# Optimization experiments

Measured on AMD Instinct MI355X. Metric: run time of the kernel, lower is better.

The kernel has to match this reference:

```python
import jax, jax.numpy as jnp
import numpy as np
from jax import lax

TSTEPS = 20
THRES = 1.0
DECAY = (2**4 - 1) / 2**4  # 0.9375


def _avgpool2(x):
    # (C,H,W) -> (C,H/2,W/2), AvgPool2d(2)
    C, H, W = x.shape
    return x.reshape(C, H // 2, 2, W // 2, 2).mean(axis=(2, 4))


def _conv(s, w):
    # s: (Cin,H,W), w: (Cout,Cin,k,k), VALID conv
    return lax.conv_general_dilated(
        s[None], w, (1, 1), 'VALID',
        dimension_numbers=('NCHW', 'OIHW', 'NCHW'))[0]


def setup_inputs() -> dict:
    key = jax.random.key(0)
    k0, k1, k2, k3, k4 = jax.random.split(key, 5)
    image = jax.random.uniform(k0, (3, 128, 128), dtype=jnp.float32)
    # kaiming_normal: std = sqrt(2/fan_in)
    w_c1 = jax.random.normal(k1, (32, 3, 5, 5), dtype=jnp.float32) * np.sqrt(2.0 / (3 * 25))
    w_c2 = jax.random.normal(k2, (64, 32, 5, 5), dtype=jnp.float32) * np.sqrt(2.0 / (32 * 25))
    w_l1 = jax.random.normal(k3, (512, 200704), dtype=jnp.float32) * np.sqrt(2.0 / 200704)
    w_l2 = jax.random.normal(k4, (10, 512), dtype=jnp.float32) * np.sqrt(2.0 / 512)
    return {"image": image, "w_c1": w_c1, "w_c2": w_c2, "w_l1": w_l1, "w_l2": w_l2}


def _lif(mempot, drive):
    # membrane update for conv/linear layers: integrate, fire, reset, decay
    mp = mempot + drive
    spk = (mp >= THRES).astype(mp.dtype)
    mp = (mp - THRES * spk) * ((1.0 - spk) * DECAY + spk)
    return mp, spk


def reference(image, w_c1, w_c2, w_l1, w_l2):
    img = _avgpool2(image)  # (3,64,64)
    f32 = jnp.float32
    carry0 = (
        jnp.zeros((3, 64, 64), f32),    # mempot input
        jnp.zeros((32, 60, 60), f32),   # mempot conv1
        jnp.zeros((64, 56, 56), f32),   # mempot conv2
        jnp.zeros((512,), f32),         # mempot linear1
        jnp.zeros((10,), f32),          # mempot linear2
        jnp.zeros((32, 60, 60), f32),   # conv1 spikes from previous step
        jnp.zeros((64, 56, 56), f32),   # conv2 spikes from previous step
        jnp.zeros((512,), f32),         # linear1 spikes from previous step
    )

    def step(carry, _):
        mp_in, mp_c1, mp_c2, mp_l1, mp_l2, sp_c1, sp_c2, sp_l1 = carry
        # input layer: integrate-and-fire, no decay
        mp_in = mp_in + img
        s_in = (mp_in >= THRES).astype(f32)
        mp_in = mp_in - THRES * s_in
        # conv1 consumes current input spikes
        mp_c1, ns_c1 = _lif(mp_c1, _conv(s_in, w_c1))
        # conv2 consumes conv1 spikes from previous timestep
        mp_c2, ns_c2 = _lif(mp_c2, _conv(sp_c1, w_c2))
        # flatten consumes conv2 spikes from previous timestep
        s_f = sp_c2.reshape(-1)  # (200704,)
        mp_l1, ns_l1 = _lif(mp_l1, w_l1 @ s_f)
        # linear2 consumes linear1 spikes from previous timestep
        mp_l2, ns_l2 = _lif(mp_l2, w_l2 @ sp_l1)
        return (mp_in, mp_c1, mp_c2, mp_l1, mp_l2, ns_c1, ns_c2, ns_l1), ns_l2

    _, out = lax.scan(step, carry0, None, length=TSTEPS)
    # original returns spikes of shape (tsteps+1, 10); row 0 stays zero
    return jnp.concatenate([jnp.zeros((1, 10), f32), out], axis=0)
```

## Files before the change

### kernel.cpp

```cpp
#include <hip/hip_runtime.h>
#include <hip/hip_bf16.h>

#define THRES 1.0f
#define DECAY 0.9375f

#define OFF_SIN    0u
#define OFF_D1     245760u
#define OFF_SC1    2549760u
#define OFF_D2     4853760u
#define OFF_MASK   8667136u
#define OFF_PART   8867840u
#define OFF_Z      8935936u

__global__ void k_input(const float* __restrict__ image, float* __restrict__ s_in) {
    int idx = blockIdx.x * 256 + threadIdx.x;
    if (idx >= 12288) return;
    int c = idx >> 12;
    int p = idx & 4095;
    int y = p >> 6, x = p & 63;
    const float* b = image + c * 16384 + (2 * y) * 128 + 2 * x;
    float v = ((b[0] + b[1]) + (b[128] + b[129])) * 0.25f;
    float mp = 0.f;
    for (int t = 0; t < 20; ++t) {
        mp += v;
        float s = (mp >= THRES) ? 1.f : 0.f;
        s_in[t * 12288 + idx] = s;
        mp -= s;
    }
}

__global__ void k_conv1(const float* __restrict__ s_in, const float* __restrict__ w_c1,
                        float* __restrict__ D1) {
    int task = blockIdx.x * 256 + threadIdx.x;
    if (task >= 57600) return;
    int xc = task % 6;
    int tmp = task / 6;
    int y = tmp % 60; tmp /= 60;
    int og = tmp % 8;
    int t  = tmp / 8;
    int o0 = og * 4, x0 = xc * 10;
    float acc[4][10];
    #pragma unroll
    for (int o = 0; o < 4; ++o)
        #pragma unroll
        for (int x = 0; x < 10; ++x) acc[o][x] = 0.f;
    const float* inb = s_in + t * 12288;
    for (int c = 0; c < 3; ++c)
        for (int ky = 0; ky < 5; ++ky) {
            float in[14];
            const float* row = inb + c * 4096 + (y + ky) * 64 + x0;
            #pragma unroll
            for (int i = 0; i < 14; ++i) in[i] = row[i];
            #pragma unroll
            for (int kx = 0; kx < 5; ++kx)
                #pragma unroll
                for (int o = 0; o < 4; ++o) {
                    float w = w_c1[((o0 + o) * 3 + c) * 25 + ky * 5 + kx];
                    #pragma unroll
                    for (int x = 0; x < 10; ++x) acc[o][x] += in[x + kx] * w;
                }
        }
    #pragma unroll
    for (int o = 0; o < 4; ++o)
        #pragma unroll
        for (int x = 0; x < 10; ++x)
            D1[((t * 32 + o0 + o) * 60 + y) * 60 + x0 + x] = acc[o][x];
}

__global__ void k_lif1(const float* __restrict__ D1, float* __restrict__ s_c1) {
    int idx = blockIdx.x * 256 + threadIdx.x;
    if (idx >= 115200) return;
    float mp = 0.f;
    for (int t = 0; t < 20; ++t) {
        mp += D1[t * 115200 + idx];
        float s = (mp >= THRES) ? 1.f : 0.f;
        s_c1[t * 115200 + idx] = s;
        mp = (s != 0.f) ? (mp - THRES) : mp * DECAY;
    }
}

__global__ void k_conv2(const float* __restrict__ s_c1, const float* __restrict__ w_c2,
                        float* __restrict__ D2) {
    int task = blockIdx.x * 256 + threadIdx.x;
    if (task >= 119168) return;
    int xc = task % 7;
    int tmp = task / 7;
    int y = tmp % 56; tmp /= 56;
    int og = tmp % 16;
    int tp = tmp / 16;
    int o0 = og * 4, x0 = xc * 8;
    float acc[4][8];
    #pragma unroll
    for (int o = 0; o < 4; ++o)
        #pragma unroll
        for (int x = 0; x < 8; ++x) acc[o][x] = 0.f;
    const float* inb = s_c1 + tp * 115200;
    for (int c = 0; c < 32; ++c)
        #pragma unroll
        for (int ky = 0; ky < 5; ++ky) {
            float in[12];
            const float* row = inb + c * 3600 + (y + ky) * 60 + x0;
            #pragma unroll
            for (int i = 0; i < 12; ++i) in[i] = row[i];
            #pragma unroll
            for (int kx = 0; kx < 5; ++kx)
                #pragma unroll
                for (int o = 0; o < 4; ++o) {
                    float w = w_c2[((o0 + o) * 32 + c) * 25 + ky * 5 + kx];
                    #pragma unroll
                    for (int x = 0; x < 8; ++x) acc[o][x] += in[x + kx] * w;
                }
        }
    #pragma unroll
    for (int o = 0; o < 4; ++o)
        #pragma unroll
        for (int x = 0; x < 8; ++x)
            D2[((tp * 64 + o0 + o) * 56 + y) * 56 + x0 + x] = acc[o][x];
}

__global__ void k_lif2(const float* __restrict__ D2, unsigned int* __restrict__ mask) {
    int idx = blockIdx.x * 256 + threadIdx.x;
    if (idx >= 200704) return;
    float mp = 0.f;
    unsigned int m = 0u;
    for (int u = 1; u < 20; ++u) {
        mp += D2[(u - 1) * 200704 + idx];
        float s = (mp >= THRES) ? 1.f : 0.f;
        if (s != 0.f) m |= (1u << u);
        mp = (s != 0.f) ? (mp - THRES) : mp * DECAY;
    }
    mask[idx] = m;
}

__global__ void __launch_bounds__(256) k_gemm(const float* __restrict__ W,
                                              const unsigned int* __restrict__ mask,
                                              float* __restrict__ partials) {
    int rg = blockIdx.x / 7, js = blockIdx.x % 7;
    int i0 = rg * 4;
    size_t j0 = (size_t)js * 28672;
    int tid = threadIdx.x;
    float acc[4][19];
    #pragma unroll
    for (int r = 0; r < 4; ++r)
        #pragma unroll
        for (int t = 0; t < 19; ++t) acc[r][t] = 0.f;

    const float* W0 = W + (size_t)(i0 + 0) * 200704 + j0;
    const float* W1 = W + (size_t)(i0 + 1) * 200704 + j0;
    const float* W2 = W + (size_t)(i0 + 2) * 200704 + j0;
    const float* W3 = W + (size_t)(i0 + 3) * 200704 + j0;
    const unsigned int* M = mask + j0;

    for (int it = 0; it < 28; ++it) {
        int j = (it * 256 + tid) * 4;
        uint4  m4 = *(const uint4*)(M + j);
        float4 a0 = *(const float4*)(W0 + j);
        float4 a1 = *(const float4*)(W1 + j);
        float4 a2 = *(const float4*)(W2 + j);
        float4 a3 = *(const float4*)(W3 + j);
        unsigned int mm[4] = {m4.x, m4.y, m4.z, m4.w};
        float w0a[4] = {a0.x, a0.y, a0.z, a0.w};
        float w1a[4] = {a1.x, a1.y, a1.z, a1.w};
        float w2a[4] = {a2.x, a2.y, a2.z, a2.w};
        float w3a[4] = {a3.x, a3.y, a3.z, a3.w};
        #pragma unroll
        for (int jj = 0; jj < 4; ++jj) {
            unsigned int m = mm[jj];
            float v0 = w0a[jj], v1 = w1a[jj], v2 = w2a[jj], v3 = w3a[jj];
            #pragma unroll
            for (int t = 0; t < 19; ++t) {
                float s = (float)((m >> t) & 1u);
                acc[0][t] += v0 * s;
                acc[1][t] += v1 * s;
                acc[2][t] += v2 * s;
                acc[3][t] += v3 * s;
            }
        }
    }

    __shared__ float red[4][76];
    int wv = tid >> 6, ln = tid & 63;
    #pragma unroll
    for (int r = 0; r < 4; ++r)
        #pragma unroll
        for (int t = 0; t < 19; ++t) {
            float v = acc[r][t];
            v += __shfl_xor(v, 32);
            v += __shfl_xor(v, 16);
            v += __shfl_xor(v, 8);
            v += __shfl_xor(v, 4);
            v += __shfl_xor(v, 2);
            v += __shfl_xor(v, 1);
            if (ln == 0) red[wv][r * 19 + t] = v;
        }
    __syncthreads();
    if (tid < 76)
        partials[(size_t)blockIdx.x * 76 + tid] =
            red[0][tid] + red[1][tid] + red[2][tid] + red[3][tid];
}

__global__ void k_reduce(const float* __restrict__ partials, float* __restrict__ Z) {
    int idx = blockIdx.x * 256 + threadIdx.x;
    if (idx >= 9728) return;
    int i = idx / 19, k = idx % 19;
    int rg = i >> 2, r = i & 3;
    float s = 0.f;
    for (int js = 0; js < 7; ++js)
        s += partials[(size_t)(rg * 7 + js) * 76 + r * 19 + k];
    Z[idx] = s;
}

__global__ void k_head(const float* __restrict__ Z, const float* __restrict__ w_l2,
                       float* __restrict__ out) {
    __shared__ float sl1[20][512];
    __shared__ float d2[20][10];
    int tid = threadIdx.x;
    {
        float mp = 0.f;
        sl1[0][tid] = 0.f;
        for (int u = 1; u < 20; ++u) {
            mp += Z[tid * 19 + (u - 1)];
            float s = (mp >= THRES) ? 1.f : 0.f;
            sl1[u][tid] = s;
            mp = (s != 0.f) ? (mp - THRES) : mp * DECAY;
        }
    }
    __syncthreads();
    int wv = tid >> 6, ln = tid & 63;
    for (int task = wv; task < 190; task += 8) {
        int u = task / 10 + 1;
        int o = task % 10;
        float p = 0.f;
        for (int ii = ln; ii < 512; ii += 64) p += w_l2[o * 512 + ii] * sl1[u - 1][ii];
        p += __shfl_xor(p, 32);
        p += __shfl_xor(p, 16);
        p += __shfl_xor(p, 8);
        p += __shfl_xor(p, 4);
        p += __shfl_xor(p, 2);
        p += __shfl_xor(p, 1);
        if (ln == 0) d2[u][o] = p;
    }
    __syncthreads();
    if (tid < 10) {
        out[tid] = 0.f;
        out[10 + tid] = 0.f;
        float mp = 0.f;
        for (int u = 1; u < 20; ++u) {
            mp += d2[u][tid];
            float s = (mp >= THRES) ? 1.f : 0.f;
            out[(u + 1) * 10 + tid] = s;
            mp = (s != 0.f) ? (mp - THRES) : mp * DECAY;
        }
    }
}

extern "C" void kernel_launch(void* const* d_in, const int* in_sizes, int n_in,
                              void* d_out, int out_size, void* d_ws, size_t ws_size,
                              hipStream_t stream) {
    const float* image = (const float*)d_in[0];
    const float* w_c1  = (const float*)d_in[1];
    const float* w_c2  = (const float*)d_in[2];
    const float* w_l1  = (const float*)d_in[3];
    const float* w_l2  = (const float*)d_in[4];
    float* out = (float*)d_out;
    float* ws  = (float*)d_ws;

    float*        s_in  = ws + OFF_SIN;
    float*        D1    = ws + OFF_D1;
    float*        s_c1  = ws + OFF_SC1;
    float*        D2    = ws + OFF_D2;
    unsigned int* mask  = (unsigned int*)(ws + OFF_MASK);
    float*        part  = ws + OFF_PART;
    float*        Z     = ws + OFF_Z;

    k_input <<<48,  256, 0, stream>>>(image, s_in);
    k_conv1 <<<225, 256, 0, stream>>>(s_in, w_c1, D1);
    k_lif1  <<<450, 256, 0, stream>>>(D1, s_c1);
    k_conv2 <<<466, 256, 0, stream>>>(s_c1, w_c2, D2);
    k_lif2  <<<784, 256, 0, stream>>>(D2, mask);
    k_gemm  <<<896, 256, 0, stream>>>(w_l1, mask, part);
    k_reduce<<<38,  256, 0, stream>>>(part, Z);
    k_head  <<<1,   512, 0, stream>>>(Z, w_l2, out);
}
```

Baseline: 729.9 us.

## Split conv output channels across more threads, widen GEMM rows, fuse reduce into head

Both conv kernels now compute 2 output channels per thread instead of 4, doubling the thread count to expose more parallelism and cut per-thread register use. The spike-GEMM now processes 8 weight rows per block over half as many columns, so each mask load is reused across more rows. The separate partial-sum reduction kernel is removed and its work folded into the single-block head kernel, saving a launch. The 152 accumulators per thread in the GEMM raise register pressure and may cause spills. The head now performs a serial 14-way reduction per neuron, and the larger partials buffer assumes enough workspace.

After: 961.2 us. 1.32x slower.

```diff
diff --git a/kernel.cpp b/kernel.cpp
--- a/kernel.cpp
+++ b/kernel.cpp
@@ -10,7 +10,6 @@
 #define OFF_D2     4853760u
 #define OFF_MASK   8667136u
 #define OFF_PART   8867840u
-#define OFF_Z      8935936u
 
 __global__ void k_input(const float* __restrict__ image, float* __restrict__ s_in) {
     int idx = blockIdx.x * 256 + threadIdx.x;
@@ -32,20 +31,21 @@
 __global__ void k_conv1(const float* __restrict__ s_in, const float* __restrict__ w_c1,
                         float* __restrict__ D1) {
     int task = blockIdx.x * 256 + threadIdx.x;
-    if (task >= 57600) return;
+    if (task >= 115200) return;
     int xc = task % 6;
     int tmp = task / 6;
     int y = tmp % 60; tmp /= 60;
-    int og = tmp % 8;
-    int t  = tmp / 8;
-    int o0 = og * 4, x0 = xc * 10;
-    float acc[4][10];
-    #pragma unroll
-    for (int o = 0; o < 4; ++o)
+    int og = tmp % 16;
+    int t  = tmp / 16;
+    int o0 = og * 2, x0 = xc * 10;
+    float acc[2][10];
+    #pragma unroll
+    for (int o = 0; o < 2; ++o)
         #pragma unroll
         for (int x = 0; x < 10; ++x) acc[o][x] = 0.f;
     const float* inb = s_in + t * 12288;
     for (int c = 0; c < 3; ++c)
+        #pragma unroll
         for (int ky = 0; ky < 5; ++ky) {
             float in[14];
             const float* row = inb + c * 4096 + (y + ky) * 64 + x0;
@@ -54,14 +54,14 @@
             #pragma unroll
             for (int kx = 0; kx < 5; ++kx)
                 #pragma unroll
-                for (int o = 0; o < 4; ++o) {
+                for (int o = 0; o < 2; ++o) {
                     float w = w_c1[((o0 + o) * 3 + c) * 25 + ky * 5 + kx];
                     #pragma unroll
                     for (int x = 0; x < 10; ++x) acc[o][x] += in[x + kx] * w;
                 }
         }
     #pragma unroll
-    for (int o = 0; o < 4; ++o)
+    for (int o = 0; o < 2; ++o)
         #pragma unroll
         for (int x = 0; x < 10; ++x)
             D1[((t * 32 + o0 + o) * 60 + y) * 60 + x0 + x] = acc[o][x];
@@ -82,16 +82,15 @@
 __global__ void k_conv2(const float* __restrict__ s_c1, const float* __restrict__ w_c2,
                         float* __restrict__ D2) {
     int task = blockIdx.x * 256 + threadIdx.x;
-    if (task >= 119168) return;
     int xc = task % 7;
     int tmp = task / 7;
     int y = tmp % 56; tmp /= 56;
-    int og = tmp % 16;
-    int tp = tmp / 16;
-    int o0 = og * 4, x0 = xc * 8;
-    float acc[4][8];
-    #pragma unroll
-    for (int o = 0; o < 4; ++o)
+    int og = tmp % 32;
+    int tp = tmp / 32;
+    int o0 = og * 2, x0 = xc * 8;
+    float acc[2][8];
+    #pragma unroll
+    for (int o = 0; o < 2; ++o)
         #pragma unroll
         for (int x = 0; x < 8; ++x) acc[o][x] = 0.f;
     const float* inb = s_c1 + tp * 115200;
@@ -105,14 +104,14 @@
             #pragma unroll
             for (int kx = 0; kx < 5; ++kx)
                 #pragma unroll
-                for (int o = 0; o < 4; ++o) {
+                for (int o = 0; o < 2; ++o) {
                     float w = w_c2[((o0 + o) * 32 + c) * 25 + ky * 5 + kx];
                     #pragma unroll
                     for (int x = 0; x < 8; ++x) acc[o][x] += in[x + kx] * w;
                 }
         }
     #pragma unroll
-    for (int o = 0; o < 4; ++o)
+    for (int o = 0; o < 2; ++o)
         #pragma unroll
         for (int x = 0; x < 8; ++x)
             D2[((tp * 64 + o0 + o) * 56 + y) * 56 + x0 + x] = acc[o][x];
@@ -135,53 +134,48 @@
 __global__ void __launch_bounds__(256) k_gemm(const float* __restrict__ W,
                                               const unsigned int* __restrict__ mask,
                                               float* __restrict__ partials) {
-    int rg = blockIdx.x / 7, js = blockIdx.x % 7;
-    int i0 = rg * 4;
-    size_t j0 = (size_t)js * 28672;
+    int rg = blockIdx.x / 14, js = blockIdx.x % 14;
+    int i0 = rg * 8;
+    size_t j0 = (size_t)js * 14336;
     int tid = threadIdx.x;
-    float acc[4][19];
-    #pragma unroll
-    for (int r = 0; r < 4; ++r)
+    float acc[8][19];
+    #pragma unroll
+    for (int r = 0; r < 8; ++r)
         #pragma unroll
         for (int t = 0; t < 19; ++t) acc[r][t] = 0.f;
 
-    const float* W0 = W + (size_t)(i0 + 0) * 200704 + j0;
-    const float* W1 = W + (size_t)(i0 + 1) * 200704 + j0;
-    const float* W2 = W + (size_t)(i0 + 2) * 200704 + j0;
-    const float* W3 = W + (size_t)(i0 + 3) * 200704 + j0;
+    const float* Wb = W + (size_t)i0 * 200704 + j0;
     const unsigned int* M = mask + j0;
 
-    for (int it = 0; it < 28; ++it) {
+    for (int it = 0; it < 14; ++it) {
         int j = (it * 256 + tid) * 4;
-        uint4  m4 = *(const uint4*)(M + j);
-        float4 a0 = *(const float4*)(W0 + j);
-        float4 a1 = *(const float4*)(W1 + j);
-        float4 a2 = *(const float4*)(W2 + j);
-        float4 a3 = *(const float4*)(W3 + j);
+        uint4 m4 = *(const uint4*)(M + j);
+        float4 a[8];
+        #pragma unroll
+        for (int r = 0; r < 8; ++r)
+            a[r] = *(const float4*)(Wb + (size_t)r * 200704 + j);
+        float av[8][4];
+        #pragma unroll
+        for (int r = 0; r < 8; ++r) {
+            av[r][0] = a[r].x; av[r][1] = a[r].y; av[r][2] = a[r].z; av[r][3] = a[r].w;
+        }
         unsigned int mm[4] = {m4.x, m4.y, m4.z, m4.w};
-        float w0a[4] = {a0.x, a0.y, a0.z, a0.w};
-        float w1a[4] = {a1.x, a1.y, a1.z, a1.w};
-        float w2a[4] = {a2.x, a2.y, a2.z, a2.w};
-        float w3a[4] = {a3.x, a3.y, a3.z, a3.w};
         #pragma unroll
         for (int jj = 0; jj < 4; ++jj) {
             unsigned int m = mm[jj];
-            float v0 = w0a[jj], v1 = w1a[jj], v2 = w2a[jj], v3 = w3a[jj];
             #pragma unroll
             for (int t = 0; t < 19; ++t) {
                 float s = (float)((m >> t) & 1u);
-                acc[0][t] += v0 * s;
-                acc[1][t] += v1 * s;
-                acc[2][t] += v2 * s;
-                acc[3][t] += v3 * s;
+                #pragma unroll
+                for (int r = 0; r < 8; ++r) acc[r][t] += av[r][jj] * s;
             }
         }
     }
 
-    __shared__ float red[4][76];
+    __shared__ float red[4][152];
     int wv = tid >> 6, ln = tid & 63;
     #pragma unroll
-    for (int r = 0; r < 4; ++r)
+    for (int r = 0; r < 8; ++r)
         #pragma unroll
         for (int t = 0; t < 19; ++t) {
             float v = acc[r][t];
@@ -194,32 +188,30 @@
             if (ln == 0) red[wv][r * 19 + t] = v;
         }
     __syncthreads();
-    if (tid < 76)
-        partials[(size_t)blockIdx.x * 76 + tid] =
+    if (tid < 152)
+        partials[(size_t)blockIdx.x * 152 + tid] =
             red[0][tid] + red[1][tid] + red[2][tid] + red[3][tid];
 }
 
-__global__ void k_reduce(const float* __restrict__ partials, float* __restrict__ Z) {
-    int idx = blockIdx.x * 256 + threadIdx.x;
-    if (idx >= 9728) return;
-    int i = idx / 19, k = idx % 19;
-    int rg = i >> 2, r = i & 3;
-    float s = 0.f;
-    for (int js = 0; js < 7; ++js)
-        s += partials[(size_t)(rg * 7 + js) * 76 + r * 19 + k];
-    Z[idx] = s;
-}
-
-__global__ void k_head(const float* __restrict__ Z, const float* __restrict__ w_l2,
+__global__ void k_head(const float* __restrict__ partials, const float* __restrict__ w_l2,
                        float* __restrict__ out) {
     __shared__ float sl1[20][512];
-    __shared__ float d2[20][10];
+    __shared__ float d2s[20][10];
     int tid = threadIdx.x;
+    int rg = tid >> 3, r = tid & 7;
+    float z[19];
+    #pragma unroll
+    for (int k = 0; k < 19; ++k) {
+        float s = 0.f;
+        for (int js = 0; js < 14; ++js)
+            s += partials[(size_t)(rg * 14 + js) * 152 + r * 19 + k];
+        z[k] = s;
+    }
     {
         float mp = 0.f;
         sl1[0][tid] = 0.f;
         for (int u = 1; u < 20; ++u) {
-            mp += Z[tid * 19 + (u - 1)];
+            mp += z[u - 1];
             float s = (mp >= THRES) ? 1.f : 0.f;
             sl1[u][tid] = s;
             mp = (s != 0.f) ? (mp - THRES) : mp * DECAY;
@@ -238,7 +230,7 @@
         p += __shfl_xor(p, 4);
         p += __shfl_xor(p, 2);
         p += __shfl_xor(p, 1);
-        if (ln == 0) d2[u][o] = p;
+        if (ln == 0) d2s[u][o] = p;
     }
     __syncthreads();
     if (tid < 10) {
@@ -246,7 +238,7 @@
         out[10 + tid] = 0.f;
         float mp = 0.f;
         for (int u = 1; u < 20; ++u) {
-            mp += d2[u][tid];
+            mp += d2s[u][tid];
             float s = (mp >= THRES) ? 1.f : 0.f;
             out[(u + 1) * 10 + tid] = s;
             mp = (s != 0.f) ? (mp - THRES) : mp * DECAY;
@@ -271,14 +263,12 @@
     float*        D2    = ws + OFF_D2;
     unsigned int* mask  = (unsigned int*)(ws + OFF_MASK);
     float*        part  = ws + OFF_PART;
-    float*        Z     = ws + OFF_Z;
 
     k_input <<<48,  256, 0, stream>>>(image, s_in);
-    k_conv1 <<<225, 256, 0, stream>>>(s_in, w_c1, D1);
+    k_conv1 <<<450, 256, 0, stream>>>(s_in, w_c1, D1);
     k_lif1  <<<450, 256, 0, stream>>>(D1, s_c1);
-    k_conv2 <<<466, 256, 0, stream>>>(s_c1, w_c2, D2);
+    k_conv2 <<<931, 256, 0, stream>>>(s_c1, w_c2, D2);
     k_lif2  <<<784, 256, 0, stream>>>(D2, mask);
     k_gemm  <<<896, 256, 0, stream>>>(w_l1, mask, part);
-    k_reduce<<<38,  256, 0, stream>>>(part, Z);
-    k_head  <<<1,   512, 0, stream>>>(Z, w_l2, out);
-}
+    k_head  <<<1,   512, 0, stream>>>(part, w_l2, out);
+}
```
